# Optimization experiments

Hardware: AMD Instinct MI355X
Metric: run time of the kernel (lower is better)

Reference implementation:

```python
import jax, jax.numpy as jnp
import numpy as np

N_POINTS = 9  # config.n_points
EPS = 1e-12
# corner offsets for the 8 trilinear neighbors, loop order (i,j,k) matches the torch code
CORNERS = jnp.array([[i, j, k] for i in (0, 1) for j in (0, 1) for k in (0, 1)], dtype=jnp.float32)  # [8,3]


def setup_inputs() -> dict:
    key = jax.random.key(0)
    k1, k2, k3 = jax.random.split(key, 3)
    b, h, w = 1, 240, 320
    X = Y = Z = 320
    # depth in [1, 4) meters
    depth = 1.0 + 3.0 * jax.random.uniform(k1, (b, h, w), dtype=jnp.float32)
    fx = fy = 300.0
    cx, cy = w / 2.0, h / 2.0
    intrinsics = jnp.array([[[fx, 0.0, cx], [0.0, fy, cy], [0.0, 0.0, 1.0]]], dtype=jnp.float32)
    extrinsics = jnp.eye(4, dtype=jnp.float32)[None]  # camera at world origin
    volume = jax.random.normal(k2, (X, Y, Z), dtype=jnp.float32)
    weights = jax.random.uniform(k3, (X, Y, Z), dtype=jnp.float32)
    origin = jnp.array([-2.0, -2.0, 0.0], dtype=jnp.float32)
    resolution = jnp.float32(4.0 / 320.0)  # 4m cube -> 320 voxels
    return dict(depth=depth, extrinsics=extrinsics, intrinsics=intrinsics,
                volume=volume, weights=weights, origin=origin, resolution=resolution)


def _compute_coordinates(depth, extrinsics, intrinsics):
    # unproject the depth map to world-space points, matching Extractor.compute_coordinates
    b, h, w = depth.shape
    xx, yy = jnp.meshgrid(jnp.arange(h, dtype=depth.dtype), jnp.arange(w, dtype=depth.dtype), indexing='ij')
    zz = depth.reshape(b, h * w)  # [b,n]
    # points_p = (u*z, v*z, z) with u=col index (yy), v=row index (xx)
    pts_p = jnp.stack([yy.reshape(-1)[None] * zz, xx.reshape(-1)[None] * zz, zz], axis=1)  # [b,3,n]
    pts_c = jnp.linalg.inv(intrinsics) @ pts_p  # [b,3,n]
    ones = jnp.ones((b, 1, h * w), depth.dtype)
    pts_c = jnp.concatenate([pts_c, ones], axis=1)  # [b,4,n]
    # (torch code uses extrinsics[:3]; with b=1 this is the full batch)
    pts_w = jnp.swapaxes(extrinsics @ pts_c, 1, 2)[:, :, :3]  # [b,n,3]
    return pts_w


def _trilinear(points, volume, wvol):
    # points: [b,n,r,3] continuous voxel coordinates
    idx = jnp.floor(points)
    center = idx + 0.5  # 'center' interpolation mode
    neighbor = jnp.sign(center - points)  # +/-1 toward nearest other cell center
    alpha = jnp.abs(points - center)  # [b,n,r,3]
    a = alpha[..., None, :]  # [b,n,r,1,3]
    w8 = jnp.prod(jnp.where(CORNERS > 0, a, 1.0 - a), axis=-1)  # [b,n,r,8]
    inds = idx[..., None, :] + CORNERS * neighbor[..., None, :]  # [b,n,r,8,3]
    shp = jnp.asarray(volume.shape, dtype=points.dtype)
    valid = jnp.all((inds >= 0) & (inds < shp), axis=-1)  # [b,n,r,8]
    ii = jnp.clip(inds, 0, shp - 1).astype(jnp.int32)
    v = volume[ii[..., 0], ii[..., 1], ii[..., 2]]
    fv = jnp.sum(jnp.where(valid, v, 0.0) * w8, axis=-1)  # [b,n,r]
    wv = wvol[ii[..., 0], ii[..., 1], ii[..., 2]]
    fw = jnp.sum(jnp.where(valid, wv, 0.0) * w8, axis=-1)  # [b,n,r]
    return fv, fw, ii, w8


def reference(depth, extrinsics, intrinsics, volume, weights, origin, resolution):
    b, h, w = depth.shape
    coords = _compute_coordinates(depth, extrinsics, intrinsics)  # [b,hw,3] world
    eye_w = extrinsics[:, :3, 3]  # [b,3]
    center_v = (coords - origin) / resolution  # voxel coords
    eye_v = (eye_w - origin) / resolution
    d = center_v - eye_v[:, None, :]
    d = d / jnp.maximum(jnp.linalg.norm(d, axis=-1, keepdims=True), EPS)  # ray directions
    k = (N_POINTS - 1) // 2
    offs = jnp.arange(-k, k + 1, dtype=depth.dtype)  # [r], bin_size=1.0
    ray_pts = center_v[:, :, None, :] + offs[None, None, :, None] * d[:, :, None, :]  # [b,hw,r,3]
    fv, fw, inds, w8 = _trilinear(ray_pts, volume, weights)
    # indices -> [b,hw,r,8,3], weights -> [b,hw,r,8] as in the torch forward
    return fv, fw, ray_pts, depth.reshape(b, h * w), inds, w8, coords
```

## Files before the change

### kernel.cpp

```cpp
#include <hip/hip_runtime.h>

#define NPIX    76800
#define WIDTH   320
#define HEIGHT  240
#define NS      9
#define NTOT    (NPIX*NS)
#define VDIM    320

#define TILE    8
#define TILES_X 40

#define BLOCK   256
#define NBLK    (NTOT / BLOCK)
#define NXCD    8
#define SWZ_Q   (NBLK / NXCD)
#define SWZ_R   (NBLK % NXCD)

#define OFF_FV  0
#define OFF_FW  691200
#define OFF_RP  1382400
#define OFF_D   3456000
#define OFF_I   3532800
#define OFF_W8  20121600
#define OFF_C   25651200

typedef float f32x4 __attribute__((ext_vector_type(4)));

__global__ __launch_bounds__(BLOCK, 8) void extractor_kernel(
    const float* __restrict__ depth,
    const float* __restrict__ extr,
    const float* __restrict__ intr,
    const float* __restrict__ vol,
    const float* __restrict__ wvol,
    const float* __restrict__ origin,
    const float* __restrict__ resolution,
    float* __restrict__ out)
{
    const int bid  = blockIdx.x;
    const int xcd  = bid & (NXCD - 1);
    const int base = bid >> 3;
    const int swz  = (xcd < SWZ_R ? xcd * (SWZ_Q + 1)
                                  : SWZ_R * (SWZ_Q + 1) + (xcd - SWZ_R) * SWZ_Q) + base;

    const int g = swz * BLOCK + threadIdx.x;
    const int q = g / 9;
    const int s = g - q * 9;

    const int tileIdx  = q >> 6;
    const int lp       = q & 63;
    const int tile_row = tileIdx / TILES_X;
    const int tile_col = tileIdx - tile_row * TILES_X;
    const int row = tile_row * TILE + (lp >> 3);
    const int col = tile_col * TILE + (lp & 7);
    const int p   = row * WIDTH + col;
    const int tid = p * NS + s;

    const float z = depth[p];

    const float a00=intr[0], a01=intr[1], a02=intr[2];
    const float a10=intr[3], a11=intr[4], a12=intr[5];
    const float a20=intr[6], a21=intr[7], a22=intr[8];
    const float det = a00*(a11*a22 - a12*a21)
                    - a01*(a10*a22 - a12*a20)
                    + a02*(a10*a21 - a11*a20);
    const float id = 1.0f / det;
    const float i00 = (a11*a22 - a12*a21)*id;
    const float i01 = (a02*a21 - a01*a22)*id;
    const float i02 = (a01*a12 - a02*a11)*id;
    const float i10 = (a12*a20 - a10*a22)*id;
    const float i11 = (a00*a22 - a02*a20)*id;
    const float i12 = (a02*a10 - a00*a12)*id;
    const float i20 = (a10*a21 - a11*a20)*id;
    const float i21 = (a01*a20 - a00*a21)*id;
    const float i22 = (a00*a11 - a01*a10)*id;

    const float up = (float)col * z;
    const float vp = (float)row * z;
    const float pcx = i00*up + i01*vp + i02*z;
    const float pcy = i10*up + i11*vp + i12*z;
    const float pcz = i20*up + i21*vp + i22*z;

    const float cwx = extr[0]*pcx + extr[1]*pcy + extr[2]*pcz  + extr[3];
    const float cwy = extr[4]*pcx + extr[5]*pcy + extr[6]*pcz  + extr[7];
    const float cwz = extr[8]*pcx + extr[9]*pcy + extr[10]*pcz + extr[11];

    const float ox = origin[0], oy = origin[1], oz = origin[2];
    const float res = resolution[0];

    const float cvx = (cwx - ox) / res;
    const float cvy = (cwy - oy) / res;
    const float cvz = (cwz - oz) / res;
    const float evx = (extr[3]  - ox) / res;
    const float evy = (extr[7]  - oy) / res;
    const float evz = (extr[11] - oz) / res;

    float dx = cvx - evx, dy = cvy - evy, dz = cvz - evz;
    const float nrm = sqrtf(dx*dx + dy*dy + dz*dz);
    const float dn  = fmaxf(nrm, 1e-12f);
    dx /= dn; dy /= dn; dz /= dn;

    const float offs = (float)(s - 4);
    const float pt[3] = { cvx + offs*dx, cvy + offs*dy, cvz + offs*dz };

    float alpha[3], nb[3], fidx[3];
    #pragma unroll
    for (int k = 0; k < 3; ++k) {
        const float f  = floorf(pt[k]);
        const float c  = f + 0.5f;
        const float df = c - pt[k];
        nb[k]    = (df > 0.0f) ? 1.0f : ((df < 0.0f) ? -1.0f : 0.0f);
        alpha[k] = fabsf(pt[k] - c);
        fidx[k]  = f;
    }

    int   lin[8];
    float wgt8[8];
    bool  valid8[8];
    float indsbuf[24];
    #pragma unroll
    for (int c = 0; c < 8; ++c) {
        float wgt = 1.0f;
        bool valid = true;
        int ii[3];
        #pragma unroll
        for (int k = 0; k < 3; ++k) {
            const float bit = ((c >> (2 - k)) & 1) ? 1.0f : 0.0f;
            wgt *= (bit > 0.0f) ? alpha[k] : (1.0f - alpha[k]);
            const float fi = fidx[k] + bit * nb[k];
            valid = valid && (fi >= 0.0f) && (fi < (float)VDIM);
            const float fc = fminf(fmaxf(fi, 0.0f), (float)(VDIM - 1));
            ii[k] = (int)fc;
            indsbuf[c*3 + k] = (float)ii[k];
        }
        lin[c]    = (ii[0]*VDIM + ii[1])*VDIM + ii[2];
        wgt8[c]   = wgt;
        valid8[c] = valid;
    }

    float v8[8], wv8[8];
    #pragma unroll
    for (int c = 0; c < 8; ++c) v8[c]  = vol[lin[c]];
    #pragma unroll
    for (int c = 0; c < 8; ++c) wv8[c] = wvol[lin[c]];

    out[OFF_RP + tid*3 + 0] = pt[0];
    out[OFF_RP + tid*3 + 1] = pt[1];
    out[OFF_RP + tid*3 + 2] = pt[2];

    f32x4* ip = reinterpret_cast<f32x4*>(out + OFF_I + tid*24);
    #pragma unroll
    for (int qd = 0; qd < 6; ++qd) {
        f32x4 v4 = { indsbuf[qd*4+0], indsbuf[qd*4+1], indsbuf[qd*4+2], indsbuf[qd*4+3] };
        ip[qd] = v4;
    }

    f32x4* wp = reinterpret_cast<f32x4*>(out + OFF_W8 + tid*8);
    f32x4 w0 = { wgt8[0], wgt8[1], wgt8[2], wgt8[3] };
    f32x4 w1 = { wgt8[4], wgt8[5], wgt8[6], wgt8[7] };
    wp[0] = w0;
    wp[1] = w1;

    if (s == 0) {
        out[OFF_D + p] = z;
        out[OFF_C + p*3 + 0] = cwx;
        out[OFF_C + p*3 + 1] = cwy;
        out[OFF_C + p*3 + 2] = cwz;
    }

    float fv = 0.0f, fw = 0.0f;
    #pragma unroll
    for (int c = 0; c < 8; ++c) {
        if (valid8[c]) { fv += v8[c] * wgt8[c]; fw += wv8[c] * wgt8[c]; }
    }
    out[OFF_FV + tid] = fv;
    out[OFF_FW + tid] = fw;
}

extern "C" void kernel_launch(void* const* d_in, const int* in_sizes, int n_in,
                              void* d_out, int out_size, void* d_ws, size_t ws_size,
                              hipStream_t stream) {
    const float* depth      = (const float*)d_in[0];
    const float* extr       = (const float*)d_in[1];
    const float* intr       = (const float*)d_in[2];
    const float* vol        = (const float*)d_in[3];
    const float* wvol       = (const float*)d_in[4];
    const float* origin     = (const float*)d_in[5];
    const float* resolution = (const float*)d_in[6];
    float* out = (float*)d_out;

    extractor_kernel<<<NBLK, BLOCK, 0, stream>>>(
        depth, extr, intr, vol, wvol, origin, resolution, out);
}
```

Measured before the change: 52.15 us.

## Stage index and weight outputs through LDS for coalesced stores, drop pixel tiling

Replaces the 8x8 pixel-tile mapping with a linear thread-to-(pixel,sample) mapping. The per-thread 96-byte index and 32-byte weight outputs are staged through a 24 KB shared buffer so each wave writes contiguous 16-byte chunks. The goal is to turn the strided vector stores into fully coalesced ones. The cost is extra LDS traffic, three block barriers, and lower occupancy (launch bounds reduced to 6 blocks per CU), while losing the spatial locality of volume gathers that the tiling gave.

```diff
diff --git a/kernel.cpp b/kernel.cpp
--- a/kernel.cpp
+++ b/kernel.cpp
@@ -2,13 +2,9 @@
 
 #define NPIX    76800
 #define WIDTH   320
-#define HEIGHT  240
 #define NS      9
 #define NTOT    (NPIX*NS)
 #define VDIM    320
-
-#define TILE    8
-#define TILES_X 40
 
 #define BLOCK   256
 #define NBLK    (NTOT / BLOCK)
@@ -26,7 +22,7 @@
 
 typedef float f32x4 __attribute__((ext_vector_type(4)));
 
-__global__ __launch_bounds__(BLOCK, 8) void extractor_kernel(
+__global__ __launch_bounds__(BLOCK, 6) void extractor_kernel(
     const float* __restrict__ depth,
     const float* __restrict__ extr,
     const float* __restrict__ intr,
@@ -36,24 +32,22 @@
     const float* __restrict__ resolution,
     float* __restrict__ out)
 {
+    __shared__ f32x4 lds4[BLOCK * 6];
+
     const int bid  = blockIdx.x;
     const int xcd  = bid & (NXCD - 1);
     const int base = bid >> 3;
     const int swz  = (xcd < SWZ_R ? xcd * (SWZ_Q + 1)
                                   : SWZ_R * (SWZ_Q + 1) + (xcd - SWZ_R) * SWZ_Q) + base;
 
-    const int g = swz * BLOCK + threadIdx.x;
-    const int q = g / 9;
-    const int s = g - q * 9;
+    const int t   = threadIdx.x;
+    const int gB  = swz * BLOCK;
+    const int tid = gB + t;
+    const int p   = tid / 9;
+    const int s   = tid - p * 9;
 
-    const int tileIdx  = q >> 6;
-    const int lp       = q & 63;
-    const int tile_row = tileIdx / TILES_X;
-    const int tile_col = tileIdx - tile_row * TILES_X;
-    const int row = tile_row * TILE + (lp >> 3);
-    const int col = tile_col * TILE + (lp & 7);
-    const int p   = row * WIDTH + col;
-    const int tid = p * NS + s;
+    const int row = p / WIDTH;
+    const int col = p - row * WIDTH;
 
     const float z = depth[p];
 
@@ -146,20 +140,6 @@
     out[OFF_RP + tid*3 + 0] = pt[0];
     out[OFF_RP + tid*3 + 1] = pt[1];
     out[OFF_RP + tid*3 + 2] = pt[2];
-
-    f32x4* ip = reinterpret_cast<f32x4*>(out + OFF_I + tid*24);
-    #pragma unroll
-    for (int qd = 0; qd < 6; ++qd) {
-        f32x4 v4 = { indsbuf[qd*4+0], indsbuf[qd*4+1], indsbuf[qd*4+2], indsbuf[qd*4+3] };
-        ip[qd] = v4;
-    }
-
-    f32x4* wp = reinterpret_cast<f32x4*>(out + OFF_W8 + tid*8);
-    f32x4 w0 = { wgt8[0], wgt8[1], wgt8[2], wgt8[3] };
-    f32x4 w1 = { wgt8[4], wgt8[5], wgt8[6], wgt8[7] };
-    wp[0] = w0;
-    wp[1] = w1;
-
     if (s == 0) {
         out[OFF_D + p] = z;
         out[OFF_C + p*3 + 0] = cwx;
@@ -174,6 +154,27 @@
     }
     out[OFF_FV + tid] = fv;
     out[OFF_FW + tid] = fw;
+
+    #pragma unroll
+    for (int c = 0; c < 6; ++c) {
+        f32x4 v4 = { indsbuf[c*4+0], indsbuf[c*4+1], indsbuf[c*4+2], indsbuf[c*4+3] };
+        lds4[t*6 + c] = v4;
+    }
+    __syncthreads();
+    f32x4* outI = reinterpret_cast<f32x4*>(out + OFF_I) + gB*6;
+    #pragma unroll
+    for (int it = 0; it < 6; ++it)
+        outI[it*BLOCK + t] = lds4[it*BLOCK + t];
+    __syncthreads();
+
+    f32x4 w0 = { wgt8[0], wgt8[1], wgt8[2], wgt8[3] };
+    f32x4 w1 = { wgt8[4], wgt8[5], wgt8[6], wgt8[7] };
+    lds4[t*2 + 0] = w0;
+    lds4[t*2 + 1] = w1;
+    __syncthreads();
+    f32x4* outW = reinterpret_cast<f32x4*>(out + OFF_W8) + gB*2;
+    outW[t]         = lds4[t];
+    outW[BLOCK + t] = lds4[BLOCK + t];
 }
 
 extern "C" void kernel_launch(void* const* d_in, const int* in_sizes, int n_in,
```

New measurement: 45.87 us. -12.1%, faster.
